# Kernel optimization log

Measured on AMD Instinct MI355X. Metric: run time of the kernel, lower is better.

Reference implementation:

```python
import jax, jax.numpy as jnp
import numpy as np

V, N, D = 3, 200000, 128   # views, n_embedding, embedding_dim
B, K = 32768, 10           # batch_size, negative_sampling_size
TOTAL = 65536              # total training pairs per view


def setup_inputs() -> dict:
    key = jax.random.key(0)
    ks = jax.random.split(key, 8)
    return {
        "count": 0,
        "shuffle_indices": jax.random.randint(ks[0], (V, TOTAL), 0, TOTAL),
        "nodes_idx": jax.random.randint(ks[1], (V, TOTAL), 0, N),
        "neigh_idx": jax.random.randint(ks[2], (V, TOTAL), 0, N),
        "neg_idx1": jax.random.randint(ks[3], (V, B, K), 0, N),
        "neg_idx2": jax.random.randint(ks[4], (V, V, B, K), 0, N),
        "neg_idx3": jax.random.randint(ks[5], (V, V, B, K), 0, N),
        "node_W": jax.random.normal(ks[6], (V, N, D), jnp.float32),
        "neigh_W": jax.random.normal(ks[7], (V, N, D), jnp.float32),
        "hyp1": jnp.ones((1,), jnp.float32),
        "hyp2": jnp.ones((1,), jnp.float32),
    }


def _sgns_term(ctx_pos, neg_table, neg_idx, center):
    # ctx_pos: [B,D] positive context embeddings; center: [B,D]; neg_idx: [B,K]
    pos = jax.nn.log_sigmoid(jnp.sum(ctx_pos * center, axis=-1)).mean()
    neg_e = neg_table[neg_idx]                                   # [B,K,D] gather
    neg = jax.nn.log_sigmoid(-jnp.einsum('bkd,bd->bk', neg_e, center)).sum(1).mean(0)
    return pos + neg


def reference(count, shuffle_indices, nodes_idx, neigh_idx,
              neg_idx1, neg_idx2, neg_idx3, node_W, neigh_W, hyp1, hyp2):
    sh = shuffle_indices[:, count:count + B]                     # [V,B]
    nodes_sel = jnp.take_along_axis(nodes_idx, sh, axis=1)       # [V,B]
    neigh_sel = jnp.take_along_axis(neigh_idx, sh, axis=1)       # [V,B]
    ar = jnp.arange(V)[:, None]
    node_e = node_W[ar, nodes_sel]                               # [V,B,D]
    neigh_e = neigh_W[ar, neigh_sel]                             # [V,B,D]

    # cost1: within-view SGNS (neigh vs node)
    cost1 = [_sgns_term(neigh_e[i], neigh_W[i], neg_idx1[i], node_e[i])
             for i in range(V)]
    # cost2: cross-view node-node alignment
    cost2 = [hyp1[0] * _sgns_term(node_W[j][nodes_sel[i]], node_W[j],
                                  neg_idx2[j, i], node_e[i])
             for j in range(V) for i in range(V) if i != j]
    # cost3: cross-view neigh-node alignment
    cost3 = [hyp2[0] * _sgns_term(neigh_W[j][neigh_sel[i]], neigh_W[j],
                                  neg_idx3[j, i], node_e[i])
             for j in range(V) for i in range(V) if i != j]

    return -(jnp.mean(jnp.stack(cost1))
             + sum(cost2) / len(cost2)
             + sum(cost3) / len(cost3)) / 3.0
```

## Files before the change

### kernel.cpp

```cpp
#include <hip/hip_runtime.h>

#define V_   3
#define N_   200000
#define D_   128
#define B_   32768
#define K_   10
#define TOT_ 65536

constexpr int BLOCKS_PER_TERM = 512;
constexpr int ROWS_PER_BLOCK  = B_ / BLOCKS_PER_TERM;
constexpr int WAVES_PER_BLOCK = 4;
constexpr int ROWS_PER_WAVE   = ROWS_PER_BLOCK / WAVES_PER_BLOCK;
constexpr int GROUPS_PER_WAVE = 4;
constexpr int ITERS           = ROWS_PER_WAVE / GROUPS_PER_WAVE;

constexpr size_t TBL_ELEMS     = (size_t)V_ * N_ * D_;
constexpr size_t FP8_TBL_BYTES = TBL_ELEMS;
constexpr size_t ACC_BYTES     = 256;
constexpr size_t WS_NEED       = ACC_BYTES + 2 * FP8_TBL_BYTES;

__device__ const int TMAP[15][3] = {
    {0, 0, 0}, {2, 1, 0}, {2, 2, 0},
    {0, 1, 1}, {2, 0, 1}, {2, 2, 1},
    {0, 2, 2}, {2, 0, 2}, {2, 1, 2},
    {1, 1, 0}, {1, 2, 0},
    {1, 0, 1}, {1, 2, 1},
    {1, 0, 2}, {1, 1, 2},
};

typedef float v2f __attribute__((ext_vector_type(2)));

template <int CTRL>
__device__ __forceinline__ float dpp_add(float v) {
    int x = __builtin_amdgcn_update_dpp(0, __float_as_int(v), CTRL, 0xF, 0xF, true);
    return v + __int_as_float(x);
}

__device__ __forceinline__ float grp_sum16(float v) {
    v = dpp_add<0xB1>(v);
    v = dpp_add<0x4E>(v);
    v = dpp_add<0x124>(v);
    v = dpp_add<0x128>(v);
    return v;
}

__device__ __forceinline__ float log_sigmoid(float x) {
    float ax = fabsf(x);
    return fminf(x, 0.f) - __logf(1.f + __expf(-ax));
}

__device__ __forceinline__ unsigned cvt4_fp8(float a, float b, float c, float d) {
    int v = __builtin_amdgcn_cvt_pk_fp8_f32(a, b, 0, false);
    v = __builtin_amdgcn_cvt_pk_fp8_f32(c, d, v, true);
    return (unsigned)v;
}
template <bool HI>
__device__ __forceinline__ v2f upk2(unsigned v) {
    return __builtin_amdgcn_cvt_pk_f32_fp8((int)v, HI);
}

__global__ __launch_bounds__(256) void cvt_fp8(const float4* __restrict__ src,
                                               uint2* __restrict__ dst, int n8)
{
    const int stride = gridDim.x * blockDim.x;
    for (int g = blockIdx.x * blockDim.x + threadIdx.x; g < n8; g += stride) {
        float4 a = src[2 * g];
        float4 b = src[2 * g + 1];
        uint2 o;
        o.x = cvt4_fp8(a.x, a.y, a.z, a.w);
        o.y = cvt4_fp8(b.x, b.y, b.z, b.w);
        dst[g] = o;
    }
}

__device__ __forceinline__ float dot8f8(v2f c0, v2f c1, v2f c2, v2f c3, uint2 n) {
    v2f n0 = upk2<false>(n.x), n1 = upk2<true>(n.x);
    v2f n2 = upk2<false>(n.y), n3 = upk2<true>(n.y);
    float s = c0.x * n0.x;
    s = fmaf(c0.y, n0.y, s);
    s = fmaf(c1.x, n1.x, s);
    s = fmaf(c1.y, n1.y, s);
    s = fmaf(c2.x, n2.x, s);
    s = fmaf(c2.y, n2.y, s);
    s = fmaf(c3.x, n3.x, s);
    s = fmaf(c3.y, n3.y, s);
    return s;
}

__global__ __launch_bounds__(256) void sgns_fp8(
    const int*   __restrict__ countp,
    const int*   __restrict__ shuffle,
    const int*   __restrict__ nodes_idx,
    const int*   __restrict__ neigh_idx,
    const int*   __restrict__ neg1,
    const int*   __restrict__ neg2,
    const int*   __restrict__ neg3,
    const uint2* __restrict__ nodeT,
    const uint2* __restrict__ neighT,
    float*       __restrict__ acc)
{
    const int slot = blockIdx.x / BLOCKS_PER_TERM;
    const int blk  = blockIdx.x % BLOCKS_PER_TERM;
    const int wave = threadIdx.x >> 6;
    const int lane = threadIdx.x & 63;
    const int grp  = lane >> 4;
    const int lw   = lane & 15;
    const int count = countp[0];

    const int type = TMAP[slot][0];
    const int i    = TMAP[slot][1];
    const int j    = TMAP[slot][2];

    const int*   negBase;
    const uint2* negTable;
    if (type == 0)      { negTable = neighT + (size_t)i * N_ * 16; negBase = neg1 + (size_t)i * B_ * K_; }
    else if (type == 1) { negTable = nodeT  + (size_t)j * N_ * 16; negBase = neg2 + (size_t)(j * V_ + i) * B_ * K_; }
    else                { negTable = neighT + (size_t)j * N_ * 16; negBase = neg3 + (size_t)(j * V_ + i) * B_ * K_; }

    float wsum = 0.f;
    const int rowbase = blk * ROWS_PER_BLOCK + wave * ROWS_PER_WAVE;

    for (int r = 0; r < ITERS; ++r) {
        const int b  = rowbase + r * GROUPS_PER_WAVE + grp;
        const int sh = shuffle[i * TOT_ + count + b];
        const int ns = nodes_idx[i * TOT_ + sh];

        uint2 c8 = nodeT[((size_t)i * N_ + ns) * 16 + lw];
        v2f c0 = upk2<false>(c8.x), c1 = upk2<true>(c8.x);
        v2f c2 = upk2<false>(c8.y), c3 = upk2<true>(c8.y);

        const uint2* xrow;
        if (type == 0) {
            int gs = neigh_idx[i * TOT_ + sh];
            xrow = neighT + ((size_t)i * N_ + gs) * 16;
        } else if (type == 1) {
            xrow = nodeT + ((size_t)j * N_ + ns) * 16;
        } else {
            int gs = neigh_idx[i * TOT_ + sh];
            xrow = neighT + ((size_t)j * N_ + gs) * 16;
        }
        uint2 x8 = xrow[lw];

        int myidx = (lw < K_) ? negBase[(size_t)b * K_ + lw] : 0;

        float rowacc = log_sigmoid(grp_sum16(dot8f8(c0, c1, c2, c3, x8)));
#pragma unroll
        for (int k = 0; k < K_; ++k) {
            int nk = __shfl(myidx, (lane & 48) | k, 64);
            uint2 n8v = negTable[(size_t)nk * 16 + lw];
            rowacc += log_sigmoid(-grp_sum16(dot8f8(c0, c1, c2, c3, n8v)));
        }
        wsum += rowacc;
    }

    wsum += __shfl_xor(wsum, 16, 64);
    wsum += __shfl_xor(wsum, 32, 64);

    __shared__ float part[WAVES_PER_BLOCK];
    if (lane == 0) part[wave] = wsum;
    __syncthreads();
    if (threadIdx.x == 0) {
        float s = part[0] + part[1] + part[2] + part[3];
        atomicAdd(&acc[type], s);
    }
}

__device__ __forceinline__ float dot8(float4 a0, float4 a1, float4 b0, float4 b1) {
    float s = a0.x * b0.x;
    s = fmaf(a0.y, b0.y, s);
    s = fmaf(a0.z, b0.z, s);
    s = fmaf(a0.w, b0.w, s);
    s = fmaf(a1.x, b1.x, s);
    s = fmaf(a1.y, b1.y, s);
    s = fmaf(a1.z, b1.z, s);
    s = fmaf(a1.w, b1.w, s);
    return s;
}

__global__ __launch_bounds__(256) void sgns_f32(
    const int*   __restrict__ countp,
    const int*   __restrict__ shuffle,
    const int*   __restrict__ nodes_idx,
    const int*   __restrict__ neigh_idx,
    const int*   __restrict__ neg1,
    const int*   __restrict__ neg2,
    const int*   __restrict__ neg3,
    const float* __restrict__ node_W,
    const float* __restrict__ neigh_W,
    float*       __restrict__ acc)
{
    const int slot = blockIdx.x / BLOCKS_PER_TERM;
    const int blk  = blockIdx.x % BLOCKS_PER_TERM;
    const int wave = threadIdx.x >> 6;
    const int lane = threadIdx.x & 63;
    const int grp  = lane >> 4;
    const int lw   = lane & 15;
    const int count = countp[0];

    const int type = TMAP[slot][0];
    const int i    = TMAP[slot][1];
    const int j    = TMAP[slot][2];

    const int*   negBase;
    const float* negTable;
    if (type == 0)      { negTable = neigh_W + (size_t)i * N_ * D_; negBase = neg1 + (size_t)i * B_ * K_; }
    else if (type == 1) { negTable = node_W  + (size_t)j * N_ * D_; negBase = neg2 + (size_t)(j * V_ + i) * B_ * K_; }
    else                { negTable = neigh_W + (size_t)j * N_ * D_; negBase = neg3 + (size_t)(j * V_ + i) * B_ * K_; }

    float wsum = 0.f;
    const int rowbase = blk * ROWS_PER_BLOCK + wave * ROWS_PER_WAVE;

    for (int r = 0; r < ITERS; ++r) {
        const int b  = rowbase + r * GROUPS_PER_WAVE + grp;
        const int sh = shuffle[i * TOT_ + count + b];
        const int ns = nodes_idx[i * TOT_ + sh];

        const float* crow = node_W + ((size_t)i * N_ + ns) * (size_t)D_;
        float4 c0 = *(const float4*)(crow + lw * 4);
        float4 c1 = *(const float4*)(crow + 64 + lw * 4);

        const float* xrow;
        if (type == 0) {
            int gs = neigh_idx[i * TOT_ + sh];
            xrow = neigh_W + ((size_t)i * N_ + gs) * (size_t)D_;
        } else if (type == 1) {
            xrow = node_W + ((size_t)j * N_ + ns) * (size_t)D_;
        } else {
            int gs = neigh_idx[i * TOT_ + sh];
            xrow = neigh_W + ((size_t)j * N_ + gs) * (size_t)D_;
        }
        float4 x0 = *(const float4*)(xrow + lw * 4);
        float4 x1 = *(const float4*)(xrow + 64 + lw * 4);

        int myidx = (lw < K_) ? negBase[(size_t)b * K_ + lw] : 0;

        float rowacc = log_sigmoid(grp_sum16(dot8(c0, c1, x0, x1)));
#pragma unroll
        for (int k = 0; k < K_; ++k) {
            int nk = __shfl(myidx, (lane & 48) | k, 64);
            const float* nrow = negTable + (size_t)nk * (size_t)D_;
            float4 n0 = *(const float4*)(nrow + lw * 4);
            float4 n1 = *(const float4*)(nrow + 64 + lw * 4);
            rowacc += log_sigmoid(-grp_sum16(dot8(c0, c1, n0, n1)));
        }
        wsum += rowacc;
    }

    wsum += __shfl_xor(wsum, 16, 64);
    wsum += __shfl_xor(wsum, 32, 64);

    __shared__ float part[WAVES_PER_BLOCK];
    if (lane == 0) part[wave] = wsum;
    __syncthreads();
    if (threadIdx.x == 0) {
        float s = part[0] + part[1] + part[2] + part[3];
        atomicAdd(&acc[type], s);
    }
}

__global__ void finalize_kernel(const float* __restrict__ acc,
                                const float* __restrict__ hyp1,
                                const float* __restrict__ hyp2,
                                float* __restrict__ out)
{
    const float invB = 1.0f / (float)B_;
    float s1 = acc[0], s2 = acc[1], s3 = acc[2];
    out[0] = -(s1 * (invB / 9.0f) + hyp1[0] * s2 * (invB / 18.0f) + hyp2[0] * s3 * (invB / 18.0f));
}

extern "C" void kernel_launch(void* const* d_in, const int* in_sizes, int n_in,
                              void* d_out, int out_size, void* d_ws, size_t ws_size,
                              hipStream_t stream)
{
    const int*   countp    = (const int*)d_in[0];
    const int*   shuffle   = (const int*)d_in[1];
    const int*   nodes_idx = (const int*)d_in[2];
    const int*   neigh_idx = (const int*)d_in[3];
    const int*   neg1      = (const int*)d_in[4];
    const int*   neg2      = (const int*)d_in[5];
    const int*   neg3      = (const int*)d_in[6];
    const float* node_W    = (const float*)d_in[7];
    const float* neigh_W   = (const float*)d_in[8];
    const float* hyp1      = (const float*)d_in[9];
    const float* hyp2      = (const float*)d_in[10];

    float* acc = (float*)d_ws;
    (void)hipMemsetAsync(acc, 0, 3 * sizeof(float), stream);

    dim3 block(256);

    if (ws_size >= WS_NEED) {
        uint2* nodeT  = (uint2*)((char*)d_ws + ACC_BYTES);
        uint2* neighT = (uint2*)((char*)d_ws + ACC_BYTES + FP8_TBL_BYTES);
        const int n8 = (int)(TBL_ELEMS / 8);
        cvt_fp8<<<4096, block, 0, stream>>>((const float4*)node_W,  nodeT,  n8);
        cvt_fp8<<<4096, block, 0, stream>>>((const float4*)neigh_W, neighT, n8);
        sgns_fp8<<<dim3(15 * BLOCKS_PER_TERM), block, 0, stream>>>(
            countp, shuffle, nodes_idx, neigh_idx, neg1, neg2, neg3,
            (const uint2*)nodeT, (const uint2*)neighT, acc);
    } else {
        sgns_f32<<<dim3(15 * BLOCKS_PER_TERM), block, 0, stream>>>(
            countp, shuffle, nodes_idx, neigh_idx, neg1, neg2, neg3,
            node_W, neigh_W, acc);
    }

    finalize_kernel<<<1, 1, 0, stream>>>(acc, hyp1, hyp2, (float*)d_out);
}
```

Baseline: 299.7 us.

## Merge fp8 conversions, fold accumulator zeroing, batch negative-row loads before math

```diff
diff --git a/kernel.cpp b/kernel.cpp
--- a/kernel.cpp
+++ b/kernel.cpp
@@ -59,32 +59,36 @@
     return __builtin_amdgcn_cvt_pk_f32_fp8((int)v, HI);
 }
 
-__global__ __launch_bounds__(256) void cvt_fp8(const float4* __restrict__ src,
-                                               uint2* __restrict__ dst, int n8)
-{
+__global__ __launch_bounds__(256) void cvt_fp8_both(
+    const float4* __restrict__ srcA, const float4* __restrict__ srcB,
+    uint2* __restrict__ dstA, uint2* __restrict__ dstB,
+    float* __restrict__ acc, int n8)
+{
+    if (blockIdx.x == 0 && threadIdx.x < 8) acc[threadIdx.x] = 0.f;
     const int stride = gridDim.x * blockDim.x;
-    for (int g = blockIdx.x * blockDim.x + threadIdx.x; g < n8; g += stride) {
-        float4 a = src[2 * g];
-        float4 b = src[2 * g + 1];
+    const int tot = 2 * n8;
+    for (int g = blockIdx.x * blockDim.x + threadIdx.x; g < tot; g += stride) {
+        const float4* s;
+        uint2* d;
+        int gi;
+        if (g < n8) { s = srcA; d = dstA; gi = g; }
+        else        { s = srcB; d = dstB; gi = g - n8; }
+        float4 a = s[2 * gi];
+        float4 b = s[2 * gi + 1];
         uint2 o;
         o.x = cvt4_fp8(a.x, a.y, a.z, a.w);
         o.y = cvt4_fp8(b.x, b.y, b.z, b.w);
-        dst[g] = o;
-    }
-}
-
-__device__ __forceinline__ float dot8f8(v2f c0, v2f c1, v2f c2, v2f c3, uint2 n) {
-    v2f n0 = upk2<false>(n.x), n1 = upk2<true>(n.x);
-    v2f n2 = upk2<false>(n.y), n3 = upk2<true>(n.y);
-    float s = c0.x * n0.x;
-    s = fmaf(c0.y, n0.y, s);
-    s = fmaf(c1.x, n1.x, s);
-    s = fmaf(c1.y, n1.y, s);
-    s = fmaf(c2.x, n2.x, s);
-    s = fmaf(c2.y, n2.y, s);
-    s = fmaf(c3.x, n3.x, s);
-    s = fmaf(c3.y, n3.y, s);
-    return s;
+        d[gi] = o;
+    }
+}
+
+__device__ __forceinline__ float dotv(v2f c0, v2f c1, v2f c2, v2f c3, uint2 n) {
+    v2f a0 = c0 * upk2<false>(n.x);
+    v2f a1 = c1 * upk2<true>(n.x);
+    a0 += c2 * upk2<false>(n.y);
+    a1 += c3 * upk2<true>(n.y);
+    v2f a = a0 + a1;
+    return a.x + a.y;
 }
 
 __global__ __launch_bounds__(256) void sgns_fp8(
@@ -126,8 +130,6 @@
         const int ns = nodes_idx[i * TOT_ + sh];
 
         uint2 c8 = nodeT[((size_t)i * N_ + ns) * 16 + lw];
-        v2f c0 = upk2<false>(c8.x), c1 = upk2<true>(c8.x);
-        v2f c2 = upk2<false>(c8.y), c3 = upk2<true>(c8.y);
 
         const uint2* xrow;
         if (type == 0) {
@@ -143,12 +145,20 @@
 
         int myidx = (lw < K_) ? negBase[(size_t)b * K_ + lw] : 0;
 
-        float rowacc = log_sigmoid(grp_sum16(dot8f8(c0, c1, c2, c3, x8)));
+        uint2 nv[K_];
 #pragma unroll
         for (int k = 0; k < K_; ++k) {
             int nk = __shfl(myidx, (lane & 48) | k, 64);
-            uint2 n8v = negTable[(size_t)nk * 16 + lw];
-            rowacc += log_sigmoid(-grp_sum16(dot8f8(c0, c1, c2, c3, n8v)));
+            nv[k] = negTable[(size_t)nk * 16 + lw];
+        }
+
+        v2f c0 = upk2<false>(c8.x), c1 = upk2<true>(c8.x);
+        v2f c2 = upk2<false>(c8.y), c3 = upk2<true>(c8.y);
+
+        float rowacc = log_sigmoid(grp_sum16(dotv(c0, c1, c2, c3, x8)));
+#pragma unroll
+        for (int k = 0; k < K_; ++k) {
+            rowacc += log_sigmoid(-grp_sum16(dotv(c0, c1, c2, c3, nv[k])));
         }
         wsum += rowacc;
     }
@@ -285,20 +295,19 @@
     const float* hyp2      = (const float*)d_in[10];
 
     float* acc = (float*)d_ws;
-    (void)hipMemsetAsync(acc, 0, 3 * sizeof(float), stream);
-
     dim3 block(256);
 
     if (ws_size >= WS_NEED) {
         uint2* nodeT  = (uint2*)((char*)d_ws + ACC_BYTES);
         uint2* neighT = (uint2*)((char*)d_ws + ACC_BYTES + FP8_TBL_BYTES);
         const int n8 = (int)(TBL_ELEMS / 8);
-        cvt_fp8<<<4096, block, 0, stream>>>((const float4*)node_W,  nodeT,  n8);
-        cvt_fp8<<<4096, block, 0, stream>>>((const float4*)neigh_W, neighT, n8);
+        cvt_fp8_both<<<8192, block, 0, stream>>>((const float4*)node_W, (const float4*)neigh_W,
+                                                 nodeT, neighT, acc, n8);
         sgns_fp8<<<dim3(15 * BLOCKS_PER_TERM), block, 0, stream>>>(
             countp, shuffle, nodes_idx, neigh_idx, neg1, neg2, neg3,
             (const uint2*)nodeT, (const uint2*)neighT, acc);
     } else {
+        (void)hipMemsetAsync(acc, 0, 3 * sizeof(float), stream);
         sgns_f32<<<dim3(15 * BLOCKS_PER_TERM), block, 0, stream>>>(
             countp, shuffle, nodes_idx, neigh_idx, neg1, neg2, neg3,
             node_W, neigh_W, acc);
```

After: 286.2 us. 1.05x faster.
